# Performance work log

Hardware: AMD Instinct MI355X
Metric: run time of the kernel (lower is better)

Reference implementation:

```python
import jax, jax.numpy as jnp
import numpy as np

N_USERS = 100000
N_MOVIES = 20000
E = 1000000
D_USER = 128
D_MOVIE = 404
HID = 256
OUT = 128


def setup_inputs() -> dict:
    key = jax.random.key(0)
    ks = jax.random.split(key, 20)
    s = 0.05
    inp = {
        'x_user': jax.random.normal(ks[0], (N_USERS, D_USER), jnp.float32),
        'x_movie': jax.random.normal(ks[1], (N_MOVIES, D_MOVIE), jnp.float32),
        'edge_src': jax.random.randint(ks[2], (E,), 0, N_USERS, jnp.int32),
        'edge_dst': jax.random.randint(ks[3], (E,), 0, N_MOVIES, jnp.int32),
        # layer 1, relation user-rates->movie: lin_l (on aggregated user msgs, with bias), lin_r (root, no bias)
        'w1_rm_l': jax.random.normal(ks[4], (D_USER, HID), jnp.float32) * s,
        'b1_rm': jnp.zeros((HID,), jnp.float32),
        'w1_rm_r': jax.random.normal(ks[5], (D_MOVIE, HID), jnp.float32) * s,
        # layer 1, relation movie-rev_rates->user
        'w1_mu_l': jax.random.normal(ks[6], (D_MOVIE, HID), jnp.float32) * s,
        'b1_mu': jnp.zeros((HID,), jnp.float32),
        'w1_mu_r': jax.random.normal(ks[7], (D_USER, HID), jnp.float32) * s,
        # layer 2, relation user-rates->movie
        'w2_rm_l': jax.random.normal(ks[8], (HID, OUT), jnp.float32) * s,
        'b2_rm': jnp.zeros((OUT,), jnp.float32),
        'w2_rm_r': jax.random.normal(ks[9], (HID, OUT), jnp.float32) * s,
        # layer 2, relation movie-rev_rates->user
        'w2_mu_l': jax.random.normal(ks[10], (HID, OUT), jnp.float32) * s,
        'b2_mu': jnp.zeros((OUT,), jnp.float32),
        'w2_mu_r': jax.random.normal(ks[11], (HID, OUT), jnp.float32) * s,
    }
    return inp


def _seg_mean(msgs, dst, n_dst):
    # mean-aggregate edge messages [E, d] into destination nodes [n_dst, d]
    s = jax.ops.segment_sum(msgs, dst, num_segments=n_dst)
    cnt = jax.ops.segment_sum(jnp.ones((dst.shape[0], 1), msgs.dtype), dst, num_segments=n_dst)
    return s / jnp.maximum(cnt, 1.0)


def _sage(x_src, x_dst, src, dst, n_dst, w_l, b_l, w_r):
    # PyG SAGEConv (mean aggr): lin_l(mean_{j->i} x_j) + lin_r(x_i)
    agg = _seg_mean(x_src[src], dst, n_dst)
    return agg @ w_l + b_l + x_dst @ w_r


def reference(x_user, x_movie, edge_src, edge_dst,
              w1_rm_l, b1_rm, w1_rm_r, w1_mu_l, b1_mu, w1_mu_r,
              w2_rm_l, b2_rm, w2_rm_r, w2_mu_l, b2_mu, w2_mu_r):
    # layer 1 (HeteroConv sum aggr is trivial: one relation per dst type) + relu
    h_movie = jax.nn.relu(_sage(x_user, x_movie, edge_src, edge_dst, N_MOVIES, w1_rm_l, b1_rm, w1_rm_r))
    h_user = jax.nn.relu(_sage(x_movie, x_user, edge_dst, edge_src, N_USERS, w1_mu_l, b1_mu, w1_mu_r))
    # layer 2 (no relu, matching the torch module)
    out_movie = _sage(h_user, h_movie, edge_src, edge_dst, N_MOVIES, w2_rm_l, b2_rm, w2_rm_r)
    out_user = _sage(h_movie, h_user, edge_dst, edge_src, N_USERS, w2_mu_l, b2_mu, w2_mu_r)
    return (out_movie, out_user)
```

## Files before the change

kernel.cpp:

```cpp
#include <hip/hip_runtime.h>
#include <cstddef>
#include <cstdint>

#define E_EDGES 1000000
#define NU 100000
#define NM 20000
#define DU 128
#define DM 404
#define HIDDIM 256
#define OUTDIM 128
#define XMW 544

typedef short bf8_t __attribute__((ext_vector_type(8)));
typedef float f32x4 __attribute__((ext_vector_type(4)));
typedef unsigned short u16x8 __attribute__((ext_vector_type(8)));

__device__ __forceinline__ float b2f(unsigned short u) {
  union { unsigned int i; float f; } x; x.i = ((unsigned int)u) << 16; return x.f;
}
__device__ __forceinline__ unsigned short f2b(float f) {
  union { float f; unsigned int i; } x; x.f = f;
  unsigned int r = x.i + 0x7FFFu + ((x.i >> 16) & 1u);
  return (unsigned short)(r >> 16);
}

#define GLOAD_LDS16(gp, lp)                                                      \
  __builtin_amdgcn_global_load_lds(                                              \
      (const __attribute__((address_space(1))) unsigned int*)(gp),               \
      (__attribute__((address_space(3))) unsigned int*)(lp), 16, 0, 0)

#define HISTB 977
__global__ __launch_bounds__(256) void hist_kernel(
    const int* __restrict__ esrc, const int* __restrict__ edst,
    int* __restrict__ deg_u, int* __restrict__ deg_m,
    int* __restrict__ rank_u, int* __restrict__ rank_m) {
  int e4 = blockIdx.x * 256 + threadIdx.x;
  if (e4 >= E_EDGES / 4) return;
  int4 s4 = reinterpret_cast<const int4*>(esrc)[e4];
  int4 d4 = reinterpret_cast<const int4*>(edst)[e4];
  int4 ru, rm;
  ru.x = atomicAdd(&deg_u[s4.x], 1);
  ru.y = atomicAdd(&deg_u[s4.y], 1);
  ru.z = atomicAdd(&deg_u[s4.z], 1);
  ru.w = atomicAdd(&deg_u[s4.w], 1);
  rm.x = atomicAdd(&deg_m[d4.x], 1);
  rm.y = atomicAdd(&deg_m[d4.y], 1);
  rm.z = atomicAdd(&deg_m[d4.z], 1);
  rm.w = atomicAdd(&deg_m[d4.w], 1);
  reinterpret_cast<int4*>(rank_u)[e4] = ru;
  reinterpret_cast<int4*>(rank_m)[e4] = rm;
}

__device__ __forceinline__ void scan_core_256(const int* __restrict__ deg,
                                              int* __restrict__ off, int n,
                                              int* wsum) {
  const int tid = threadIdx.x;
  const int lane = tid & 63;
  const int w = tid >> 6;
  int carry = 0;
  for (int base = 0; base < n; base += 4096) {
    const int i0 = base + tid * 16;
    int v[16];
    int s = 0;
    if (i0 + 16 <= n) {
#pragma unroll
      for (int q = 0; q < 4; ++q) {
        int4 t4 = *reinterpret_cast<const int4*>(&deg[i0 + q * 4]);
        v[q * 4 + 0] = t4.x; v[q * 4 + 1] = t4.y; v[q * 4 + 2] = t4.z; v[q * 4 + 3] = t4.w;
      }
    } else {
#pragma unroll
      for (int j = 0; j < 16; ++j) v[j] = (i0 + j < n) ? deg[i0 + j] : 0;
    }
#pragma unroll
    for (int j = 0; j < 16; ++j) s += v[j];
    int ws_ = s;
#pragma unroll
    for (int d = 1; d < 64; d <<= 1) {
      int t = __shfl_up(ws_, d, 64);
      if (lane >= d) ws_ += t;
    }
    if (lane == 63) wsum[w] = ws_;
    __syncthreads();
    int woff = 0, ctot = 0;
#pragma unroll
    for (int j = 0; j < 4; ++j) {
      int x = wsum[j];
      if (j < w) woff += x;
      ctot += x;
    }
    int ex = carry + woff + ws_ - s;
    if (i0 + 16 <= n) {
      int o[16];
#pragma unroll
      for (int j = 0; j < 16; ++j) { o[j] = ex; ex += v[j]; }
#pragma unroll
      for (int q = 0; q < 4; ++q)
        *reinterpret_cast<int4*>(&off[i0 + q * 4]) =
            make_int4(o[q * 4], o[q * 4 + 1], o[q * 4 + 2], o[q * 4 + 3]);
    } else {
#pragma unroll
      for (int j = 0; j < 16; ++j) {
        if (i0 + j < n) off[i0 + j] = ex;
        ex += v[j];
      }
    }
    carry += ctot;
    __syncthreads();
  }
  if (tid == 0) off[n] = carry;
}

#define PRA 3200000
#define PRB 5280000
#define PRC 5722368
__global__ __launch_bounds__(256) void scanprep_kernel(
    const int* __restrict__ deg_m, int* __restrict__ off_m,
    const int* __restrict__ deg_u, int* __restrict__ off_u,
    const float* __restrict__ x_user, unsigned short* __restrict__ xu_bf,
    const float* __restrict__ x_movie, unsigned short* __restrict__ xmcat,
    const float* __restrict__ w1_rm_l, const float* __restrict__ w1_rm_r,
    const float* __restrict__ w1_mu_l, const float* __restrict__ w1_mu_r,
    const float* __restrict__ w2_rm_l, const float* __restrict__ w2_mu_r,
    const float* __restrict__ w2_mu_l, const float* __restrict__ w2_rm_r,
    unsigned short* __restrict__ wL1, unsigned short* __restrict__ w1mur,
    unsigned short* __restrict__ wL2u, unsigned short* __restrict__ w2mul,
    unsigned short* __restrict__ w2rmr) {
  __shared__ int wsum[4];
  if (blockIdx.x == 0) { scan_core_256(deg_m, off_m, NM, wsum); return; }
  if (blockIdx.x == 1) { scan_core_256(deg_u, off_u, NU, wsum); return; }
  int j = (blockIdx.x - 2) * 256 + threadIdx.x;
  if (j < PRA) {
    float4 v = reinterpret_cast<const float4*>(x_user)[j];
    ushort4 o;
    o.x = f2b(v.x); o.y = f2b(v.y); o.z = f2b(v.z); o.w = f2b(v.w);
    reinterpret_cast<ushort4*>(xu_bf)[j] = o;
  } else if (j < PRB) {
    int q = j - PRA;
    int row = q / 104, c4 = (q % 104) * 4;
    ushort4 o;
    if (c4 < DM) {
      float4 v = *reinterpret_cast<const float4*>(&x_movie[(size_t)row * DM + c4]);
      o.x = f2b(v.x); o.y = f2b(v.y); o.z = f2b(v.z); o.w = f2b(v.w);
    } else {
      o.x = o.y = o.z = o.w = 0;
    }
    *reinterpret_cast<ushort4*>(&xmcat[(size_t)row * XMW + 128 + c4]) = o;
  } else if (j < PRC) {
    int q = j - PRB;
    if (q < 278528) {
      int n = q / 544, k = q % 544;
      float v = 0.f;
      if (n < 256) {
        if (k < 128) v = w1_rm_l[(size_t)k * 256 + n];
        else if (k < 532) v = w1_rm_r[(size_t)(k - 128) * 256 + n];
      } else {
        if (k >= 128 && k < 532) v = w1_mu_l[(size_t)(k - 128) * 256 + (n - 256)];
      }
      wL1[q] = f2b(v);
    } else if (q < 311296) {
      int p = q - 278528; int n = p / 128, k = p % 128;
      w1mur[p] = f2b(w1_mu_r[(size_t)k * 256 + n]);
    } else if (q < 376832) {
      int p = q - 311296; int n = p / 256, k = p % 256;
      float v = (n < 128) ? w2_rm_l[(size_t)k * 128 + n] : w2_mu_r[(size_t)k * 128 + (n - 128)];
      wL2u[p] = f2b(v);
    } else if (q < 409600) {
      int p = q - 376832; int n = p / 256, k = p % 256;
      w2mul[p] = f2b(w2_mu_l[(size_t)k * 128 + n]);
    } else {
      int p = q - 409600; int n = p / 256, k = p % 256;
      w2rmr[p] = f2b(w2_rm_r[(size_t)k * 128 + n]);
    }
  }
}

template <int MODE>
__device__ __forceinline__ void gemm_core(
    const unsigned short* __restrict__ A, int lda,
    const unsigned short* __restrict__ Bt, int ldb, int K,
    const unsigned short* __restrict__ elem, const float* __restrict__ bias,
    void* __restrict__ outA, int M, int bx, int by,
    unsigned short* Alds, unsigned short* Blds) {
  const int tid = threadIdx.x;
  const int w = tid >> 6, l = tid & 63;
  const int row0 = bx * 128;
  const int col0 = by * 128;
  const int wr = w >> 1, wc = w & 1;

  f32x4 acc[4][4] = {};

  int ar0 = row0 + w * 32 + (l >> 2);
  int ar1 = ar0 + 16;
  if (ar0 >= M) ar0 = M - 1;
  if (ar1 >= M) ar1 = M - 1;
  const size_t aoff0 = (size_t)ar0 * lda + (l & 3) * 8;
  const size_t aoff1 = (size_t)ar1 * lda + (l & 3) * 8;
  const int nr0 = col0 + w * 32 + (l >> 2);
  const size_t boff0 = (size_t)nr0 * ldb + (l & 3) * 8;
  const size_t boff1 = (size_t)(nr0 + 16) * ldb + (l & 3) * 8;
  unsigned short* aldsb = &Alds[w * 1024];
  unsigned short* bldsb = &Blds[w * 1024];

  for (int k0 = 0; k0 < K; k0 += 32) {
    GLOAD_LDS16(A + aoff0 + k0, aldsb);
    GLOAD_LDS16(A + aoff1 + k0, aldsb + 512);
    GLOAD_LDS16(Bt + boff0 + k0, bldsb);
    GLOAD_LDS16(Bt + boff1 + k0, bldsb + 512);
    __syncthreads();
    bf8_t af[4], bfr[4];
#pragma unroll
    for (int mi = 0; mi < 4; ++mi)
      af[mi] = *reinterpret_cast<const bf8_t*>(&Alds[(wr * 64 + mi * 16 + (l & 15)) * 32 + (l >> 4) * 8]);
#pragma unroll
    for (int nj = 0; nj < 4; ++nj)
      bfr[nj] = *reinterpret_cast<const bf8_t*>(&Blds[(wc * 64 + nj * 16 + (l & 15)) * 32 + (l >> 4) * 8]);
#pragma unroll
    for (int mi = 0; mi < 4; ++mi)
#pragma unroll
      for (int nj = 0; nj < 4; ++nj)
        acc[mi][nj] = __builtin_amdgcn_mfma_f32_16x16x32_bf16(af[mi], bfr[nj], acc[mi][nj], 0, 0, 0);
    __syncthreads();
  }

#pragma unroll
  for (int mi = 0; mi < 4; ++mi) {
    const int rbase = row0 + wr * 64 + mi * 16 + ((l >> 4) << 2);
#pragma unroll
    for (int nj = 0; nj < 4; ++nj) {
      const int col = col0 + wc * 64 + nj * 16 + (l & 15);
      float bb = 0.0f;
      if constexpr (MODE == 0 || MODE == 1 || MODE == 6) bb = bias[col];
#pragma unroll
      for (int r = 0; r < 4; ++r) {
        const int row = rbase + r;
        if (row >= M) continue;
        float v = acc[mi][nj][r] + bb;
        if constexpr (MODE == 1) v += b2f(elem[(size_t)row * 256 + col]);
        if constexpr (MODE == 0 || MODE == 1) v = fmaxf(v, 0.0f);
        if constexpr (MODE == 0 || MODE == 1 || MODE == 5) {
          ((unsigned short*)outA)[(size_t)row * 256 + col] = f2b(v);
        } else if constexpr (MODE == 2) {
          ((unsigned short*)outA)[(size_t)row * 128 + col] = f2b(v);
        } else {
          ((float*)outA)[(size_t)row * 128 + col] = v;
        }
      }
    }
  }
}

#define FILLB 977
__global__ __launch_bounds__(256) void fill_t1_kernel(
    const int* __restrict__ esrc, const int* __restrict__ edst,
    const int* __restrict__ rank_m, const int* __restrict__ rank_u,
    const int* __restrict__ off_m, const int* __restrict__ off_u,
    int* __restrict__ csr_m, int* __restrict__ csr_u,
    const unsigned short* __restrict__ A, const unsigned short* __restrict__ Bt,
    unsigned short* __restrict__ t1) {
  __shared__ unsigned short Alds[128 * 32];
  __shared__ unsigned short Blds[128 * 32];
  if (blockIdx.x < FILLB) {
    int e4 = blockIdx.x * 256 + threadIdx.x;
    if (e4 >= E_EDGES / 4) return;
    int4 s4 = reinterpret_cast<const int4*>(esrc)[e4];
    int4 d4 = reinterpret_cast<const int4*>(edst)[e4];
    int4 rm = reinterpret_cast<const int4*>(rank_m)[e4];
    int4 ru = reinterpret_cast<const int4*>(rank_u)[e4];
    csr_m[off_m[d4.x] + rm.x] = s4.x;
    csr_m[off_m[d4.y] + rm.y] = s4.y;
    csr_m[off_m[d4.z] + rm.z] = s4.z;
    csr_m[off_m[d4.w] + rm.w] = s4.w;
    csr_u[off_u[s4.x] + ru.x] = d4.x;
    csr_u[off_u[s4.y] + ru.y] = d4.y;
    csr_u[off_u[s4.z] + ru.z] = d4.z;
    csr_u[off_u[s4.w] + ru.w] = d4.w;
    return;
  }
  const int bi = blockIdx.x - FILLB;
  gemm_core<5>(A, XMW, Bt, XMW, 416, nullptr, nullptr, t1, NM,
               bi % 157, bi / 157, Alds, Blds);
}

template <int D>
__device__ __forceinline__ void gather_core(
    const unsigned short* __restrict__ table, const int* __restrict__ off,
    const int* __restrict__ idx, unsigned short* __restrict__ out,
    int n, int ostride, int bi) {
  constexpr int LPN = D / 8;
  constexpr int NPB = 256 / LPN;
  const int t = threadIdx.x;
  const int g = t / LPN;
  const int cl = (t % LPN) * 8;
  const int node = bi * NPB + g;
  if (node >= n) return;
  const int beg = off[node], end = off[node + 1];
  const float sc = 1.0f / fmaxf((float)(end - beg), 1.0f);
  float a[8] = {0, 0, 0, 0, 0, 0, 0, 0}, b[8] = {0, 0, 0, 0, 0, 0, 0, 0};
  int p = beg;
  for (; p + 3 < end; p += 4) {
    const int r0 = idx[p], r1 = idx[p + 1], r2 = idx[p + 2], r3 = idx[p + 3];
    u16x8 v0 = *reinterpret_cast<const u16x8*>(&table[(size_t)r0 * D + cl]);
    u16x8 v1 = *reinterpret_cast<const u16x8*>(&table[(size_t)r1 * D + cl]);
    u16x8 v2 = *reinterpret_cast<const u16x8*>(&table[(size_t)r2 * D + cl]);
    u16x8 v3 = *reinterpret_cast<const u16x8*>(&table[(size_t)r3 * D + cl]);
#pragma unroll
    for (int j = 0; j < 8; ++j) { a[j] += b2f(v0[j]); b[j] += b2f(v1[j]); }
#pragma unroll
    for (int j = 0; j < 8; ++j) { a[j] += b2f(v2[j]); b[j] += b2f(v3[j]); }
  }
  for (; p < end; ++p) {
    const int r0 = idx[p];
    u16x8 v0 = *reinterpret_cast<const u16x8*>(&table[(size_t)r0 * D + cl]);
#pragma unroll
    for (int j = 0; j < 8; ++j) a[j] += b2f(v0[j]);
  }
  u16x8 o;
#pragma unroll
  for (int j = 0; j < 8; ++j) o[j] = f2b((a[j] + b[j]) * sc);
  *reinterpret_cast<u16x8*>(&out[(size_t)node * ostride + cl]) = o;
}

__device__ __forceinline__ void gather_add_f32_128(
    const unsigned short* __restrict__ table, const int* __restrict__ off,
    const int* __restrict__ idx, float* __restrict__ out, int n, int bi) {
  const int t = threadIdx.x;
  const int g = t >> 4;
  const int cl = (t & 15) * 8;
  const int node = bi * 16 + g;
  if (node >= n) return;
  const int beg = off[node], end = off[node + 1];
  const float sc = 1.0f / fmaxf((float)(end - beg), 1.0f);
  float a[8] = {0, 0, 0, 0, 0, 0, 0, 0}, b[8] = {0, 0, 0, 0, 0, 0, 0, 0};
  int p = beg;
  for (; p + 3 < end; p += 4) {
    const int r0 = idx[p], r1 = idx[p + 1], r2 = idx[p + 2], r3 = idx[p + 3];
    u16x8 v0 = *reinterpret_cast<const u16x8*>(&table[(size_t)r0 * 128 + cl]);
    u16x8 v1 = *reinterpret_cast<const u16x8*>(&table[(size_t)r1 * 128 + cl]);
    u16x8 v2 = *reinterpret_cast<const u16x8*>(&table[(size_t)r2 * 128 + cl]);
    u16x8 v3 = *reinterpret_cast<const u16x8*>(&table[(size_t)r3 * 128 + cl]);
#pragma unroll
    for (int j = 0; j < 8; ++j) { a[j] += b2f(v0[j]); b[j] += b2f(v1[j]); }
#pragma unroll
    for (int j = 0; j < 8; ++j) { a[j] += b2f(v2[j]); b[j] += b2f(v3[j]); }
  }
  for (; p < end; ++p) {
    const int r0 = idx[p];
    u16x8 v0 = *reinterpret_cast<const u16x8*>(&table[(size_t)r0 * 128 + cl]);
#pragma unroll
    for (int j = 0; j < 8; ++j) a[j] += b2f(v0[j]);
  }
  float* dst = &out[(size_t)node * 128 + cl];
  float4 o0 = *reinterpret_cast<const float4*>(dst);
  float4 o1 = *reinterpret_cast<const float4*>(dst + 4);
  o0.x += (a[0] + b[0]) * sc; o0.y += (a[1] + b[1]) * sc;
  o0.z += (a[2] + b[2]) * sc; o0.w += (a[3] + b[3]) * sc;
  o1.x += (a[4] + b[4]) * sc; o1.y += (a[5] + b[5]) * sc;
  o1.z += (a[6] + b[6]) * sc; o1.w += (a[7] + b[7]) * sc;
  *reinterpret_cast<float4*>(dst) = o0;
  *reinterpret_cast<float4*>(dst + 4) = o1;
}

__global__ __launch_bounds__(256) void gatherA_kernel(
    const unsigned short* __restrict__ t1, const int* __restrict__ off_u,
    const int* __restrict__ csr_u, unsigned short* __restrict__ M1u,
    const unsigned short* __restrict__ xu, const int* __restrict__ off_m,
    const int* __restrict__ csr_m, unsigned short* __restrict__ xmcat) {
  if (blockIdx.x < 12500)
    gather_core<256>(t1, off_u, csr_u, M1u, NU, 256, blockIdx.x);
  else
    gather_core<128>(xu, off_m, csr_m, xmcat, NM, XMW, blockIdx.x - 12500);
}

__global__ __launch_bounds__(256) void gemmA_kernel(
    const unsigned short* __restrict__ xmcat, const unsigned short* __restrict__ wL1,
    const float* __restrict__ b1_rm, unsigned short* __restrict__ hm,
    const unsigned short* __restrict__ xu, const unsigned short* __restrict__ w1mur,
    const unsigned short* __restrict__ M1u, const float* __restrict__ b1_mu,
    unsigned short* __restrict__ hu) {
  __shared__ unsigned short Alds[128 * 32];
  __shared__ unsigned short Blds[128 * 32];
  if (blockIdx.x < 314) {
    int bi = blockIdx.x;
    gemm_core<0>(xmcat, XMW, wL1, XMW, XMW, nullptr, b1_rm, hm, NM,
                 bi % 157, bi / 157, Alds, Blds);
  } else {
    int bi = blockIdx.x - 314;
    gemm_core<1>(xu, 128, w1mur, 128, 128, M1u, b1_mu, hu, NU,
                 bi % 782, bi / 782, Alds, Blds);
  }
}

__global__ __launch_bounds__(256) void gemmB2_kernel(
    const unsigned short* __restrict__ hu, const unsigned short* __restrict__ w2rml,
    unsigned short* __restrict__ hul,
    const unsigned short* __restrict__ hm, const unsigned short* __restrict__ w2mul,
    unsigned short* __restrict__ t2,
    const unsigned short* __restrict__ w2mur, const float* __restrict__ b2_mu,
    float* __restrict__ out_user,
    const unsigned short* __restrict__ w2rmr, const float* __restrict__ b2_rm,
    float* __restrict__ out_movie) {
  __shared__ unsigned short Alds[128 * 32];
  __shared__ unsigned short Blds[128 * 32];
  if (blockIdx.x < 782) {
    gemm_core<2>(hu, 256, w2rml, 256, 256, nullptr, nullptr, hul, NU,
                 blockIdx.x, 0, Alds, Blds);
  } else if (blockIdx.x < 939) {
    gemm_core<2>(hm, 256, w2mul, 256, 256, nullptr, nullptr, t2, NM,
                 blockIdx.x - 782, 0, Alds, Blds);
  } else if (blockIdx.x < 1721) {
    gemm_core<6>(hu, 256, w2mur, 256, 256, nullptr, b2_mu, out_user, NU,
                 blockIdx.x - 939, 0, Alds, Blds);
  } else {
    gemm_core<6>(hm, 256, w2rmr, 256, 256, nullptr, b2_rm, out_movie, NM,
                 blockIdx.x - 1721, 0, Alds, Blds);
  }
}

__global__ __launch_bounds__(256) void gatherBC_kernel(
    const unsigned short* __restrict__ t2, const int* __restrict__ off_u,
    const int* __restrict__ csr_u, float* __restrict__ out_user,
    const unsigned short* __restrict__ hul, const int* __restrict__ off_m,
    const int* __restrict__ csr_m, float* __restrict__ out_movie) {
  if (blockIdx.x < 6250)
    gather_add_f32_128(t2, off_u, csr_u, out_user, NU, blockIdx.x);
  else
    gather_add_f32_128(hul, off_m, csr_m, out_movie, NM, blockIdx.x - 6250);
}

extern "C" void kernel_launch(void* const* d_in, const int* in_sizes, int n_in,
                              void* d_out, int out_size, void* d_ws, size_t ws_size,
                              hipStream_t stream) {
  const float* x_user  = (const float*)d_in[0];
  const float* x_movie = (const float*)d_in[1];
  const int*   esrc    = (const int*)d_in[2];
  const int*   edst    = (const int*)d_in[3];
  const float* w1_rm_l = (const float*)d_in[4];
  const float* b1_rm   = (const float*)d_in[5];
  const float* w1_rm_r = (const float*)d_in[6];
  const float* w1_mu_l = (const float*)d_in[7];
  const float* b1_mu   = (const float*)d_in[8];
  const float* w1_mu_r = (const float*)d_in[9];
  const float* w2_rm_l = (const float*)d_in[10];
  const float* b2_rm   = (const float*)d_in[11];
  const float* w2_rm_r = (const float*)d_in[12];
  const float* w2_mu_l = (const float*)d_in[13];
  const float* b2_mu   = (const float*)d_in[14];
  const float* w2_mu_r = (const float*)d_in[15];

  if (ws_size < 214240008ull) return;
  char* wsb = (char*)d_ws;
  unsigned short* xu_bf  = (unsigned short*)(wsb + 0);
  unsigned short* xmcat  = (unsigned short*)(wsb + 25600000);
  unsigned short* hm_bf  = (unsigned short*)(wsb + 47360000);
  unsigned short* t1_bf  = (unsigned short*)(wsb + 57600000);
  unsigned short* t2_bf  = (unsigned short*)(wsb + 67840000);
  unsigned short* M1u_bf = (unsigned short*)(wsb + 72960000);
  unsigned short* hul_bf = (unsigned short*)(wsb + 72960000);
  unsigned short* hu_bf  = (unsigned short*)(wsb + 149760000);
  int* rank_m = (int*)(wsb + 149760000);
  int* rank_u = (int*)(wsb + 153760000);
  unsigned short* wts = (unsigned short*)(wsb + 200960000);
  unsigned short* wL1_t   = wts;
  unsigned short* w1mur_t = wts + 278528;
  unsigned short* wL2u_t  = wts + 311296;
  unsigned short* w2mul_t = wts + 376832;
  unsigned short* w2rmr_t = wts + 409600;
  int* iw    = (int*)(wsb + 201844736);
  int* deg_m = iw;
  int* deg_u = iw + 20000;
  int* off_m = iw + 120000;
  int* off_u = iw + 140004;
  int* csr_m = iw + 240008;
  int* csr_u = iw + 1240008;

  float* out_movie = (float*)d_out;
  float* out_user  = (float*)d_out + (size_t)NM * OUTDIM;

  hipMemsetAsync(deg_m, 0, 120000 * sizeof(int), stream);
  hist_kernel<<<HISTB, 256, 0, stream>>>(esrc, edst, deg_u, deg_m, rank_u, rank_m);

  scanprep_kernel<<<2 + (PRC + 255) / 256, 256, 0, stream>>>(
      deg_m, off_m, deg_u, off_u,
      x_user, xu_bf, x_movie, xmcat,
      w1_rm_l, w1_rm_r, w1_mu_l, w1_mu_r, w2_rm_l, w2_mu_r, w2_mu_l, w2_rm_r,
      wL1_t, w1mur_t, wL2u_t, w2mul_t, w2rmr_t);

  fill_t1_kernel<<<FILLB + 314, 256, 0, stream>>>(
      esrc, edst, rank_m, rank_u, off_m, off_u, csr_m, csr_u,
      xmcat + 128, wL1_t + 256 * XMW + 128, t1_bf);

  gatherA_kernel<<<12500 + 1250, 256, 0, stream>>>(
      t1_bf, off_u, csr_u, M1u_bf, xu_bf, off_m, csr_m, xmcat);

  gemmA_kernel<<<314 + 1564, 256, 0, stream>>>(
      xmcat, wL1_t, b1_rm, hm_bf, xu_bf, w1mur_t, M1u_bf, b1_mu, hu_bf);

  gemmB2_kernel<<<1878, 256, 0, stream>>>(
      hu_bf, wL2u_t, hul_bf, hm_bf, w2mul_t, t2_bf,
      wL2u_t + 128 * 256, b2_mu, out_user, w2rmr_t, b2_rm, out_movie);

  gatherBC_kernel<<<6250 + 1250, 256, 0, stream>>>(
      t2_bf, off_u, csr_u, out_user, hul_bf, off_m, csr_m, out_movie);
}
```

Measured before the change: 463.1 us.

## Split user-side gathers into 64-column slices for cache locality

The user-side mean-aggregation gathers now split the feature dimension into 64-column slices, with separate block ranges per slice. Each block covers 32 nodes with 8 threads per node instead of full-width rows. The goal is a smaller per-pass working set of the gathered table (the movie table), so random row reads hit in L2/MALL more often. The cost is that the CSR offsets and indices are read several times, once per slice.

Result: faster. 448.9 us (-3.1%).

```diff
diff --git a/kernel.cpp b/kernel.cpp
--- a/kernel.cpp
+++ b/kernel.cpp
@@ -321,6 +321,83 @@
   *reinterpret_cast<u16x8*>(&out[(size_t)node * ostride + cl]) = o;
 }
 
+__device__ __forceinline__ void gather_slice64(
+    const unsigned short* __restrict__ table, int tstride,
+    const int* __restrict__ off, const int* __restrict__ idx,
+    unsigned short* __restrict__ out, int ostride, int n, int col0, int bi) {
+  const int t = threadIdx.x;
+  const int g = t >> 3;
+  const int cl = col0 + (t & 7) * 8;
+  const int node = bi * 32 + g;
+  if (node >= n) return;
+  const int beg = off[node], end = off[node + 1];
+  const float sc = 1.0f / fmaxf((float)(end - beg), 1.0f);
+  float a[8] = {0, 0, 0, 0, 0, 0, 0, 0}, b[8] = {0, 0, 0, 0, 0, 0, 0, 0};
+  int p = beg;
+  for (; p + 3 < end; p += 4) {
+    const int r0 = idx[p], r1 = idx[p + 1], r2 = idx[p + 2], r3 = idx[p + 3];
+    u16x8 v0 = *reinterpret_cast<const u16x8*>(&table[(size_t)r0 * tstride + cl]);
+    u16x8 v1 = *reinterpret_cast<const u16x8*>(&table[(size_t)r1 * tstride + cl]);
+    u16x8 v2 = *reinterpret_cast<const u16x8*>(&table[(size_t)r2 * tstride + cl]);
+    u16x8 v3 = *reinterpret_cast<const u16x8*>(&table[(size_t)r3 * tstride + cl]);
+#pragma unroll
+    for (int j = 0; j < 8; ++j) { a[j] += b2f(v0[j]); b[j] += b2f(v1[j]); }
+#pragma unroll
+    for (int j = 0; j < 8; ++j) { a[j] += b2f(v2[j]); b[j] += b2f(v3[j]); }
+  }
+  for (; p < end; ++p) {
+    const int r0 = idx[p];
+    u16x8 v0 = *reinterpret_cast<const u16x8*>(&table[(size_t)r0 * tstride + cl]);
+#pragma unroll
+    for (int j = 0; j < 8; ++j) a[j] += b2f(v0[j]);
+  }
+  u16x8 o;
+#pragma unroll
+  for (int j = 0; j < 8; ++j) o[j] = f2b((a[j] + b[j]) * sc);
+  *reinterpret_cast<u16x8*>(&out[(size_t)node * ostride + cl]) = o;
+}
+
+__device__ __forceinline__ void gather_add_slice64(
+    const unsigned short* __restrict__ table, int tstride,
+    const int* __restrict__ off, const int* __restrict__ idx,
+    float* __restrict__ out, int ostride, int n, int col0, int bi) {
+  const int t = threadIdx.x;
+  const int g = t >> 3;
+  const int cl = col0 + (t & 7) * 8;
+  const int node = bi * 32 + g;
+  if (node >= n) return;
+  const int beg = off[node], end = off[node + 1];
+  const float sc = 1.0f / fmaxf((float)(end - beg), 1.0f);
+  float a[8] = {0, 0, 0, 0, 0, 0, 0, 0}, b[8] = {0, 0, 0, 0, 0, 0, 0, 0};
+  int p = beg;
+  for (; p + 3 < end; p += 4) {
+    const int r0 = idx[p], r1 = idx[p + 1], r2 = idx[p + 2], r3 = idx[p + 3];
+    u16x8 v0 = *reinterpret_cast<const u16x8*>(&table[(size_t)r0 * tstride + cl]);
+    u16x8 v1 = *reinterpret_cast<const u16x8*>(&table[(size_t)r1 * tstride + cl]);
+    u16x8 v2 = *reinterpret_cast<const u16x8*>(&table[(size_t)r2 * tstride + cl]);
+    u16x8 v3 = *reinterpret_cast<const u16x8*>(&table[(size_t)r3 * tstride + cl]);
+#pragma unroll
+    for (int j = 0; j < 8; ++j) { a[j] += b2f(v0[j]); b[j] += b2f(v1[j]); }
+#pragma unroll
+    for (int j = 0; j < 8; ++j) { a[j] += b2f(v2[j]); b[j] += b2f(v3[j]); }
+  }
+  for (; p < end; ++p) {
+    const int r0 = idx[p];
+    u16x8 v0 = *reinterpret_cast<const u16x8*>(&table[(size_t)r0 * tstride + cl]);
+#pragma unroll
+    for (int j = 0; j < 8; ++j) a[j] += b2f(v0[j]);
+  }
+  float* dst = &out[(size_t)node * ostride + cl];
+  float4 o0 = *reinterpret_cast<const float4*>(dst);
+  float4 o1 = *reinterpret_cast<const float4*>(dst + 4);
+  o0.x += (a[0] + b[0]) * sc; o0.y += (a[1] + b[1]) * sc;
+  o0.z += (a[2] + b[2]) * sc; o0.w += (a[3] + b[3]) * sc;
+  o1.x += (a[4] + b[4]) * sc; o1.y += (a[5] + b[5]) * sc;
+  o1.z += (a[6] + b[6]) * sc; o1.w += (a[7] + b[7]) * sc;
+  *reinterpret_cast<float4*>(dst) = o0;
+  *reinterpret_cast<float4*>(dst + 4) = o1;
+}
+
 __device__ __forceinline__ void gather_add_f32_128(
     const unsigned short* __restrict__ table, const int* __restrict__ off,
     const int* __restrict__ idx, float* __restrict__ out, int n, int bi) {
@@ -366,10 +443,13 @@
     const int* __restrict__ csr_u, unsigned short* __restrict__ M1u,
     const unsigned short* __restrict__ xu, const int* __restrict__ off_m,
     const int* __restrict__ csr_m, unsigned short* __restrict__ xmcat) {
-  if (blockIdx.x < 12500)
-    gather_core<256>(t1, off_u, csr_u, M1u, NU, 256, blockIdx.x);
-  else
+  if (blockIdx.x < 12500) {
+    const int s = blockIdx.x / 3125;
+    const int bi = blockIdx.x % 3125;
+    gather_slice64(t1, 256, off_u, csr_u, M1u, 256, NU, s * 64, bi);
+  } else {
     gather_core<128>(xu, off_m, csr_m, xmcat, NM, XMW, blockIdx.x - 12500);
+  }
 }
 
 __global__ __launch_bounds__(256) void gemmA_kernel(
@@ -422,10 +502,13 @@
     const int* __restrict__ csr_u, float* __restrict__ out_user,
     const unsigned short* __restrict__ hul, const int* __restrict__ off_m,
     const int* __restrict__ csr_m, float* __restrict__ out_movie) {
-  if (blockIdx.x < 6250)
-    gather_add_f32_128(t2, off_u, csr_u, out_user, NU, blockIdx.x);
-  else
+  if (blockIdx.x < 6250) {
+    const int s = blockIdx.x / 3125;
+    const int bi = blockIdx.x % 3125;
+    gather_add_slice64(t2, 128, off_u, csr_u, out_user, 128, NU, s * 64, bi);
+  } else {
     gather_add_f32_128(hul, off_m, csr_m, out_movie, NM, blockIdx.x - 6250);
+  }
 }
 
 extern "C" void kernel_launch(void* const* d_in, const int* in_sizes, int n_in,
```
